# Kernel tuning notes

Hardware: AMD Instinct MI355X
Metric: run time of the kernel (lower is better)

Reference implementation:

```python
import jax, jax.numpy as jnp
import numpy as np

EPS = 1e-5

def _conv2d(x, w, b, pad):
    # NCHW conv, stride 1
    out = jax.lax.conv_general_dilated(x, w, (1, 1), [(pad, pad), (pad, pad)],
                                       dimension_numbers=('NCHW', 'OIHW', 'NCHW'))
    return out + b[None, :, None, None]

def _deform_conv2d(x, offset, mask, weight, bias, pad):
    # torchvision.ops.deform_conv2d (modulated, stride=1, dilation=1)
    B, C, H, W = x.shape
    O, _, K, _ = weight.shape
    kk = K * K
    off = offset.reshape(B, kk, 2, H, W)
    dy, dx = off[:, :, 0], off[:, :, 1]          # [B,kk,H,W]
    ki = (jnp.arange(kk) // K).astype(x.dtype)
    kj = (jnp.arange(kk) % K).astype(x.dtype)
    hh = jnp.arange(H, dtype=x.dtype)
    ww = jnp.arange(W, dtype=x.dtype)
    ys = dy + (hh[None, :, None] + ki[:, None, None] - pad)[None]  # [B,kk,H,W]
    xs = dx + (ww[None, None, :] + kj[:, None, None] - pad)[None]
    y0 = jnp.floor(ys); x0 = jnp.floor(xs)
    wy = ys - y0; wx = xs - x0
    xf = x.reshape(B, C, H * W)

    def gather(yi, xi):
        valid = ((yi >= 0) & (yi <= H - 1) & (xi >= 0) & (xi <= W - 1)).astype(x.dtype)
        yc = jnp.clip(yi, 0, H - 1).astype(jnp.int32)
        xc = jnp.clip(xi, 0, W - 1).astype(jnp.int32)
        idx = (yc * W + xc).reshape(B, -1)
        v = jax.vmap(lambda f, i: f[:, i])(xf, idx).reshape(B, C, kk, H, W)
        return v * valid[:, None]

    one = jnp.asarray(1.0, x.dtype)
    sampled = (gather(y0, x0) * ((one - wy) * (one - wx))[:, None]
               + gather(y0, x0 + 1) * ((one - wy) * wx)[:, None]
               + gather(y0 + 1, x0) * (wy * (one - wx))[:, None]
               + gather(y0 + 1, x0 + 1) * (wy * wx)[:, None])
    sampled = sampled * mask[:, None]            # modulation
    out = jnp.einsum('bckhw,ock->bohw', sampled, weight.reshape(O, C, kk))
    return out + bias[None, :, None, None]

def setup_inputs() -> dict:
    key = jax.random.key(0)
    ks = jax.random.split(key, 7)
    B, C, H, W = 8, 768, 32, 32
    x = jax.random.normal(ks[0], (B, C, H, W), jnp.float32)
    proj_w = jax.random.normal(ks[1], (768, 768, 3, 3), jnp.float32) * 0.02
    proj_b = jax.random.normal(ks[2], (768,), jnp.float32) * 0.02
    offset_w = jax.random.normal(ks[3], (18, 768, 3, 3), jnp.float32) * 0.01
    offset_b = jax.random.normal(ks[4], (18,), jnp.float32) * 0.01
    mask_w = jax.random.normal(ks[5], (9, 768, 3, 3), jnp.float32) * 0.01
    mask_b = jax.random.normal(ks[6], (9,), jnp.float32) * 0.01
    gamma = jnp.ones((768,), jnp.float32)
    beta = jnp.zeros((768,), jnp.float32)
    return {"x": x, "proj_w": proj_w, "proj_b": proj_b, "offset_w": offset_w,
            "offset_b": offset_b, "mask_w": mask_w, "mask_b": mask_b,
            "gamma": gamma, "beta": beta}

def reference(x, proj_w, proj_b, offset_w, offset_b, mask_w, mask_b, gamma, beta):
    pad = 1
    H, W = x.shape[-2], x.shape[-1]
    max_off = float(min(H, W) // 4)
    offset = jnp.clip(_conv2d(x, offset_w, offset_b, pad), -max_off, max_off)
    mask = 2.0 * jax.nn.sigmoid(_conv2d(x, mask_w, mask_b, pad))
    y = _deform_conv2d(x, offset, mask, proj_w, proj_b, pad)
    # SyncBatchNorm (training-mode batch statistics, biased var)
    mean = jnp.mean(y, axis=(0, 2, 3))
    var = jnp.var(y, axis=(0, 2, 3))
    yn = (y - mean[None, :, None, None]) * jax.lax.rsqrt(var + EPS)[None, :, None, None]
    yn = yn * gamma[None, :, None, None] + beta[None, :, None, None]
    return x + jax.nn.gelu(yn, approximate=False)
```

## Files before the change

### kernel.cpp

```cpp
#include <hip/hip_runtime.h>
#include <math.h>

typedef __attribute__((ext_vector_type(4))) float f32x4;
typedef __attribute__((ext_vector_type(8))) short s16x8;
typedef __attribute__((ext_vector_type(4))) unsigned int u32x4;
typedef unsigned short ushort_t;

#define HW   1024
#define C_IN 768
#define B_N  8

__device__ inline ushort_t f2bf(float f) {
    unsigned u = __builtin_bit_cast(unsigned, f);
    unsigned r = u + 0x7FFFu + ((u >> 16) & 1u);
    return (ushort_t)(r >> 16);
}
__device__ inline float bf2f(short s) {
    return __builtin_bit_cast(float, ((unsigned)(ushort_t)s) << 16);
}
__device__ inline void glds16(const void* g, void* l) {
    __builtin_amdgcn_global_load_lds(
        (const __attribute__((address_space(1))) unsigned*)g,
        (__attribute__((address_space(3))) unsigned*)l, 16, 0, 0);
}

__global__ __launch_bounds__(256) void prepack_xt(
    const float* __restrict__ x, ushort_t* __restrict__ xt)
{
    __shared__ ushort_t tile[64][66];
    int bid = blockIdx.x;
    int b  = bid / 192;
    int r  = bid % 192;
    int cg = r / 16, pg = r % 16;
    int c0 = cg * 64, p0 = pg * 64;
    int t = threadIdx.x;
#pragma unroll
    for (int i = 0; i < 16; ++i) {
        int idx = t + i * 256;
        int cr = idx >> 6, col = idx & 63;
        tile[cr][col] = f2bf(x[(((size_t)b * C_IN + c0 + cr) << 10) + p0 + col]);
    }
    __syncthreads();
#pragma unroll
    for (int i = 0; i < 16; ++i) {
        int idx = t + i * 256;
        int pr = idx >> 6, col = idx & 63;
        xt[((size_t)(b << 10) + p0 + pr) * C_IN + c0 + col] = tile[col][pr];
    }
}

__global__ __launch_bounds__(256) void prepack_proj(
    const float* __restrict__ pw, ushort_t* __restrict__ A)
{
    __shared__ ushort_t tile[16][584];
    int bid = blockIdx.x;
    int mf = bid / 12, cblk = bid - mf * 12;
    int t = threadIdx.x;
    const float* src = pw + (size_t)mf * 16 * 6912 + cblk * 576;
#pragma unroll
    for (int i = 0; i < 36; ++i) {
        int f = i * 256 + t;
        int orow = f / 576, col = f - orow * 576;
        tile[orow][col] = f2bf(src[(size_t)orow * 6912 + col]);
    }
    __syncthreads();
    int lane = t & 63, fi0 = t >> 6;
    for (int it = 0; it < 5; ++it) {
        int fidx = it * 4 + fi0;
        if (fidx < 18) {
            int tap = fidx >> 1, half = fidx & 1;
            int s = tap * 24 + cblk * 2 + half;
            int cl0 = half * 32 + ((lane >> 4) << 3);
            s16x8 pk;
#pragma unroll
            for (int e = 0; e < 8; ++e)
                pk[e] = (short)tile[lane & 15][(cl0 + e) * 9 + tap];
            *(s16x8*)(A + ((size_t)(s * 48 + mf) * 64 + lane) * 8) = pk;
        }
    }
}

__global__ __launch_bounds__(256) void prepack_om(
    const float* __restrict__ offw, const float* __restrict__ mskw,
    ushort_t* __restrict__ A2)
{
    int t = blockIdx.x * 256 + threadIdx.x;
    int lane = t & 63;
    int smi  = t >> 6;
    int s  = smi >> 1, mf = smi & 1;
    int oc = mf * 16 + (lane & 15);
    int k0 = s * 32 + ((lane >> 4) << 3);
    int tap = k0 / 768;
    int c   = k0 - tap * 768;
    s16x8 pk;
#pragma unroll
    for (int e = 0; e < 8; ++e) pk[e] = 0;
    if (oc < 27) {
        const float* src = (oc < 18)
            ? offw + ((size_t)oc        * 768 + c) * 9 + tap
            : mskw + ((size_t)(oc - 18) * 768 + c) * 9 + tap;
#pragma unroll
        for (int e = 0; e < 8; ++e) pk[e] = (short)f2bf(src[e * 9]);
    }
    *(s16x8*)(A2 + (size_t)smi * 512 + lane * 8) = pk;
}

__global__ __launch_bounds__(256) void offmask_mfma(
    const ushort_t* __restrict__ xt, const ushort_t* __restrict__ A2,
    const float* __restrict__ offb, const float* __restrict__ mbias,
    float* __restrict__ offs, float* __restrict__ maskb)
{
    int bid = blockIdx.x;
    int b = bid >> 5, pt = bid & 31;
    int p0 = pt << 5;
    int t = threadIdx.x, lane = t & 63, wv = t >> 6;
    int mf = wv >> 1, nf = wv & 1;
    int q = lane >> 4;
    int px = p0 + nf * 16 + (lane & 15);
    int h = px >> 5, w = px & 31;
    const char* xb = (const char*)xt + (size_t)b * (HW * 1536);
    f32x4 acc = (f32x4){0.f, 0.f, 0.f, 0.f};

    for (int tap = 0; tap < 9; ++tap) {
        int yy = h + tap / 3 - 1, xx = w + tap % 3 - 1;
        bool ok = (yy >= 0 && yy < 32 && xx >= 0 && xx < 32);
        int pos = ok ? (yy * 32 + xx) : 0;
        const char* bp = xb + (size_t)pos * 1536 + q * 16;
        for (int cs = 0; cs < 24; ++cs) {
            int s = tap * 24 + cs;
            s16x8 bf;
            if (ok) bf = *(const s16x8*)(bp + cs * 64);
            else    bf = (s16x8){0, 0, 0, 0, 0, 0, 0, 0};
            s16x8 af = *(const s16x8*)(A2 + ((size_t)(s * 2 + mf) * 64 + lane) * 8);
            acc = __builtin_amdgcn_mfma_f32_16x16x32_bf16(af, bf, acc, 0, 0, 0);
        }
    }
#pragma unroll
    for (int r = 0; r < 4; ++r) {
        int oc = mf * 16 + ((lane >> 4) << 2) + r;
        if (oc < 18) {
            float v = acc[r] + offb[oc];
            v = fminf(fmaxf(v, -8.f), 8.f);
            offs[((b * 18 + oc) << 10) + px] = v;
        } else if (oc < 27) {
            float v = acc[r] + mbias[oc - 18];
            maskb[((b * 9 + oc - 18) << 10) + px] = 2.f / (1.f + expf(-v));
        }
    }
}

__global__ __launch_bounds__(512) void sample_pack(
    const ushort_t* __restrict__ xt,
    const float* __restrict__ offs, const float* __restrict__ maskb,
    ushort_t* __restrict__ Bp)
{
    __shared__ float4 mw[9][16];
    __shared__ int4   mi[9][16];
    int bid = blockIdx.x;
    int b = bid >> 6, pxg = bid & 63;
    int px0 = pxg << 4;
    int t = threadIdx.x;

    if (t < 144) {
        int tap = t >> 4, pxl = t & 15;
        int px = px0 + pxl, h = px >> 5, w = px & 31;
        float dy = offs[((b * 18 + 2 * tap) << 10) + px];
        float dx = offs[((b * 18 + 2 * tap + 1) << 10) + px];
        float m  = maskb[((b * 9 + tap) << 10) + px];
        float ys = dy + (float)(h + tap / 3 - 1);
        float xs = dx + (float)(w + tap % 3 - 1);
        float fy = floorf(ys), fx = floorf(xs);
        float wy = ys - fy, wx = xs - fx;
        int iy0 = (int)fy, ix0 = (int)fx;
        int iy1 = iy0 + 1, ix1 = ix0 + 1;
        float vy0 = (iy0 >= 0 && iy0 < 32) ? 1.f : 0.f;
        float vy1 = (iy1 >= 0 && iy1 < 32) ? 1.f : 0.f;
        float vx0 = (ix0 >= 0 && ix0 < 32) ? 1.f : 0.f;
        float vx1 = (ix1 >= 0 && ix1 < 32) ? 1.f : 0.f;
        int cy0 = min(max(iy0, 0), 31), cx0 = min(max(ix0, 0), 31);
        int cy1 = min(max(iy1, 0), 31), cx1 = min(max(ix1, 0), 31);
        float4 wv4;
        wv4.x = (1.f - wy) * (1.f - wx) * m * vy0 * vx0;
        wv4.y = (1.f - wy) * wx         * m * vy0 * vx1;
        wv4.z = wy         * (1.f - wx) * m * vy1 * vx0;
        wv4.w = wy         * wx         * m * vy1 * vx1;
        mw[tap][pxl] = wv4;
        mi[tap][pxl] = make_int4((cy0 * 32 + cx0) * 1536, (cy0 * 32 + cx1) * 1536,
                                 (cy1 * 32 + cx0) * 1536, (cy1 * 32 + cx1) * 1536);
    }
    __syncthreads();

    int lane = t & 63, wv = t >> 6;
    int pxl = lane & 15, ko = lane >> 4;
    const char* xb = (const char*)xt + (size_t)b * (HW * 1536);

    for (int s = wv; s < 216; s += 8) {
        int tap = s / 24, cq = s - tap * 24;
        float4 w4 = mw[tap][pxl];
        int4  i4 = mi[tap][pxl];
        const char* base = xb + cq * 64 + ko * 16;
        s16x8 g0 = *(const s16x8*)(base + i4.x);
        s16x8 g1 = *(const s16x8*)(base + i4.y);
        s16x8 g2 = *(const s16x8*)(base + i4.z);
        s16x8 g3 = *(const s16x8*)(base + i4.w);
        u32x4 bw;
#pragma unroll
        for (int e2 = 0; e2 < 4; ++e2) {
            float v0 = w4.x * bf2f(g0[2 * e2])     + w4.y * bf2f(g1[2 * e2])
                     + w4.z * bf2f(g2[2 * e2])     + w4.w * bf2f(g3[2 * e2]);
            float v1 = w4.x * bf2f(g0[2 * e2 + 1]) + w4.y * bf2f(g1[2 * e2 + 1])
                     + w4.z * bf2f(g2[2 * e2 + 1]) + w4.w * bf2f(g3[2 * e2 + 1]);
            unsigned rr;
            asm("v_cvt_pk_bf16_f32 %0, %1, %2" : "=v"(rr) : "v"(v0), "v"(v1));
            bw[e2] = rr;
        }
        *(u32x4*)(Bp + ((size_t)(s * 8 + b) * 64 + pxg) * 512 + lane * 8) = bw;
    }
}

__global__ __launch_bounds__(1024, 2) void deform_gemm_lds2(
    const ushort_t* __restrict__ Amat, const ushort_t* __restrict__ Bp,
    float* __restrict__ y)
{
    __shared__ __align__(16) char Sbuf[4][20480];

    int id = blockIdx.x;
    int b = id & 7;
    int pxt = (id >> 3) & 7;
    int otile = id >> 6;
    int t = threadIdx.x, lane = t & 63, wv = t >> 6;
    int wm = wv >> 2, wn = wv & 3;

    f32x4 acc[3][2];
#pragma unroll
    for (int f = 0; f < 3; ++f)
#pragma unroll
        for (int n = 0; n < 2; ++n) acc[f][n] = (f32x4){0.f, 0.f, 0.f, 0.f};

#define CHUNK_SRC(c_, s_) ((c_) < 12                                         \
    ? (const char*)Amat + (((size_t)(s_) * 48 + otile * 12 + (c_)) << 10)    \
    : (const char*)Bp + ((((size_t)(s_) * 8 + b) * 64 + pxt * 8 + ((c_) - 12)) << 10))

#define STAGE(BUF, s_) do {                                                  \
    int c1_ = wv;                                                            \
    glds16(CHUNK_SRC(c1_, s_) + lane * 16, &Sbuf[BUF][c1_ << 10]);           \
    if (wv < 4) {                                                            \
        int c2_ = 16 + wv;                                                   \
        glds16(CHUNK_SRC(c2_, s_) + lane * 16, &Sbuf[BUF][c2_ << 10]);       \
    }                                                                        \
} while (0)

#define MFMA_PHASE(BUF) do {                                                 \
    const char* ab_ = &Sbuf[BUF][(wm * 3) << 10] + lane * 16;                \
    s16x8 a0_ = *(const s16x8*)(ab_);                                        \
    s16x8 a1_ = *(const s16x8*)(ab_ + 1024);                                 \
    s16x8 a2_ = *(const s16x8*)(ab_ + 2048);                                 \
    const char* bb_ = &Sbuf[BUF][(12 + wn * 2) << 10] + lane * 16;           \
    s16x8 b0_ = *(const s16x8*)(bb_);                                        \
    s16x8 b1_ = *(const s16x8*)(bb_ + 1024);                                 \
    acc[0][0] = __builtin_amdgcn_mfma_f32_16x16x32_bf16(a0_, b0_, acc[0][0], 0, 0, 0); \
    acc[0][1] = __builtin_amdgcn_mfma_f32_16x16x32_bf16(a0_, b1_, acc[0][1], 0, 0, 0); \
    acc[1][0] = __builtin_amdgcn_mfma_f32_16x16x32_bf16(a1_, b0_, acc[1][0], 0, 0, 0); \
    acc[1][1] = __builtin_amdgcn_mfma_f32_16x16x32_bf16(a1_, b1_, acc[1][1], 0, 0, 0); \
    acc[2][0] = __builtin_amdgcn_mfma_f32_16x16x32_bf16(a2_, b0_, acc[2][0], 0, 0, 0); \
    acc[2][1] = __builtin_amdgcn_mfma_f32_16x16x32_bf16(a2_, b1_, acc[2][1], 0, 0, 0); \
} while (0)

    STAGE(0, 0);
    STAGE(1, 1);

    for (int p = 0; p < 214; ++p) {
        int bufc = p & 3;
        STAGE((p + 2) & 3, p + 2);
        if (wv < 4) asm volatile("s_waitcnt vmcnt(4)" ::: "memory");
        else        asm volatile("s_waitcnt vmcnt(2)" ::: "memory");
        __builtin_amdgcn_s_barrier();
        __builtin_amdgcn_s_setprio(1);
        MFMA_PHASE(bufc);
        __builtin_amdgcn_s_setprio(0);
    }
    if (wv < 4) asm volatile("s_waitcnt vmcnt(2)" ::: "memory");
    else        asm volatile("s_waitcnt vmcnt(1)" ::: "memory");
    __builtin_amdgcn_s_barrier();
    MFMA_PHASE(214 & 3);
    asm volatile("s_waitcnt vmcnt(0)" ::: "memory");
    __builtin_amdgcn_s_barrier();
    MFMA_PHASE(215 & 3);

    int pxo = pxt * 128 + wn * 32 + (lane & 15);
    int obase = otile * 192 + wm * 48;
#pragma unroll
    for (int f = 0; f < 3; ++f) {
        int orow = obase + f * 16 + ((lane >> 4) << 2);
#pragma unroll
        for (int r = 0; r < 4; ++r) {
            size_t rowoff = ((size_t)(b * 768 + orow + r) << 10);
            y[rowoff + pxo]      = acc[f][0][r];
            y[rowoff + pxo + 16] = acc[f][1][r];
        }
    }
#undef CHUNK_SRC
#undef STAGE
#undef MFMA_PHASE
}

__global__ __launch_bounds__(512, 4) void deform_mfma_fused(
    const ushort_t* __restrict__ xt, const ushort_t* __restrict__ Amat,
    const float* __restrict__ offs, const float* __restrict__ maskb,
    float* __restrict__ y)
{
    __shared__ float4 meta_w[576];
    __shared__ int4   meta_i[576];
    __shared__ __align__(16) ushort_t Bs[2][64][64];

    int id = blockIdx.x;
    int b = id & 7;
    int pxt = (id >> 3) & 15;
    int otile = id >> 7;
    int p0 = pxt << 6;
    int t = threadIdx.x, lane = t & 63, wv = t >> 6;
    int wm = wv >> 1, wn = wv & 1;
    int q4 = lane >> 4;

    int bpx = wv * 8 + (lane >> 3);
    int oct = lane & 7;
    const int wchunk = (oct ^ (bpx & 7)) * 8;

    for (int i = t; i < 576; i += 512) {
        int k = i >> 6, j = i & 63;
        int hw = p0 + j, h = hw >> 5, w = hw & 31;
        float dy = offs[((b * 18 + 2 * k) << 10) + hw];
        float dx = offs[((b * 18 + 2 * k + 1) << 10) + hw];
        float m  = maskb[((b * 9 + k) << 10) + hw];
        float ys = dy + (float)(h + k / 3 - 1);
        float xs = dx + (float)(w + k % 3 - 1);
        float fy = floorf(ys), fx = floorf(xs);
        float wy = ys - fy, wx = xs - fx;
        int iy0 = (int)fy, ix0 = (int)fx;
        int iy1 = iy0 + 1, ix1 = ix0 + 1;
        float vy0 = (iy0 >= 0 && iy0 < 32) ? 1.f : 0.f;
        float vy1 = (iy1 >= 0 && iy1 < 32) ? 1.f : 0.f;
        float vx0 = (ix0 >= 0 && ix0 < 32) ? 1.f : 0.f;
        float vx1 = (ix1 >= 0 && ix1 < 32) ? 1.f : 0.f;
        int cy0 = min(max(iy0, 0), 31), cx0 = min(max(ix0, 0), 31);
        int cy1 = min(max(iy1, 0), 31), cx1 = min(max(ix1, 0), 31);
        float4 wv4;
        wv4.x = (1.f - wy) * (1.f - wx) * m * vy0 * vx0;
        wv4.y = (1.f - wy) * wx         * m * vy0 * vx1;
        wv4.z = wy         * (1.f - wx) * m * vy1 * vx0;
        wv4.w = wy         * wx         * m * vy1 * vx1;
        meta_w[i] = wv4;
        meta_i[i] = make_int4((cy0 * 32 + cx0) * 1536, (cy0 * 32 + cx1) * 1536,
                              (cy1 * 32 + cx0) * 1536, (cy1 * 32 + cx1) * 1536);
    }
    asm volatile("s_waitcnt lgkmcnt(0)" ::: "memory");
    __builtin_amdgcn_s_barrier();

    f32x4 acc[3][2];
#pragma unroll
    for (int f = 0; f < 3; ++f)
#pragma unroll
        for (int n = 0; n < 2; ++n) acc[f][n] = (f32x4){0.f, 0.f, 0.f, 0.f};

    const char* xb = (const char*)xt + (size_t)b * (HW * 1536);
    const int afrag0 = otile * 12 + wm * 3;

    s16x8 ga0, ga1, ga2, ga3, gb0, gb1, gb2, gb3;
    float4 w4a, w4b;

#define WBAR() do { asm volatile("s_waitcnt lgkmcnt(0)" ::: "memory"); \
                    __builtin_amdgcn_s_barrier(); } while (0)
#define ISSUE(G0, G1, G2, G3, W4, qq) do {                                  \
    int nt_ = (qq) / 12, nc_ = (qq) - nt_ * 12;                             \
    W4 = meta_w[nt_ * 64 + bpx];                                            \
    int4 i4_ = meta_i[nt_ * 64 + bpx];                                      \
    const char* bsrc_ = xb + nc_ * 128 + oct * 16;                          \
    G0 = *(const s16x8*)(bsrc_ + i4_.x);                                    \
    G1 = *(const s16x8*)(bsrc_ + i4_.y);                                    \
    G2 = *(const s16x8*)(bsrc_ + i4_.z);                                    \
    G3 = *(const s16x8*)(bsrc_ + i4_.w);                                    \
} while (0)
#define BUILD(G0, G1, G2, G3, W4, BUF) do {                                 \
    u32x4 bw_;                                                              \
    _Pragma("unroll")                                                       \
    for (int e2 = 0; e2 < 4; ++e2) {                                        \
        float v0_ = W4.x * bf2f(G0[2*e2])   + W4.y * bf2f(G1[2*e2])         \
                  + W4.z * bf2f(G2[2*e2])   + W4.w * bf2f(G3[2*e2]);        \
        float v1_ = W4.x * bf2f(G0[2*e2+1]) + W4.y * bf2f(G1[2*e2+1])       \
                  + W4.z * bf2f(G2[2*e2+1]) + W4.w * bf2f(G3[2*e2+1]);      \
        unsigned rr_;                                                       \
        asm("v_cvt_pk_bf16_f32 %0, %1, %2" : "=v"(rr_) : "v"(v0_), "v"(v1_)); \
        bw_[e2] = rr_;                                                      \
    }                                                                       \
    *(u32x4*)&Bs[BUF][bpx][wchunk] = bw_;                                   \
} while (0)
#define MFMA_PHASE_F(P, BUF) do {                                           \
    _Pragma("unroll")                                                       \
    for (int kk = 0; kk < 2; ++kk) {                                        \
        int s_ = 2 * (P) + kk;                                              \
        const s16x8* ap_ = (const s16x8*)(Amat +                            \
            ((size_t)(s_ * 48 + afrag0) * 64 + lane) * 8);                  \
        s16x8 a0_ = ap_[0], a1_ = ap_[64], a2_ = ap_[128];                  \
        int rc_ = ((kk * 4 + q4) ^ (lane & 7)) * 8;                         \
        s16x8 b0_ = *(const s16x8*)&Bs[BUF][wn * 32 + (lane & 15)][rc_];    \
        s16x8 b1_ = *(const s16x8*)&Bs[BUF][wn * 32 + 16 + (lane & 15)][rc_]; \
        acc[0][0] = __builtin_amdgcn_mfma_f32_16x16x32_bf16(a0_, b0_, acc[0][0], 0, 0, 0); \
        acc[0][1] = __builtin_amdgcn_mfma_f32_16x16x32_bf16(a0_, b1_, acc[0][1], 0, 0, 0); \
        acc[1][0] = __builtin_amdgcn_mfma_f32_16x16x32_bf16(a1_, b0_, acc[1][0], 0, 0, 0); \
        acc[1][1] = __builtin_amdgcn_mfma_f32_16x16x32_bf16(a1_, b1_, acc[1][1], 0, 0, 0); \
        acc[2][0] = __builtin_amdgcn_mfma_f32_16x16x32_bf16(a2_, b0_, acc[2][0], 0, 0, 0); \
        acc[2][1] = __builtin_amdgcn_mfma_f32_16x16x32_bf16(a2_, b1_, acc[2][1], 0, 0, 0); \
    }                                                                       \
} while (0)

    ISSUE(ga0, ga1, ga2, ga3, w4a, 0);
    ISSUE(gb0, gb1, gb2, gb3, w4b, 1);
    BUILD(ga0, ga1, ga2, ga3, w4a, 0);
    WBAR();
    for (int pp = 0; pp < 54; ++pp) {
        int pe = 2 * pp;
        if (pp < 53) ISSUE(ga0, ga1, ga2, ga3, w4a, pe + 2);
        MFMA_PHASE_F(pe, 0);
        BUILD(gb0, gb1, gb2, gb3, w4b, 1);
        WBAR();
        int po = pe + 1;
        if (pp < 53) ISSUE(gb0, gb1, gb2, gb3, w4b, po + 2);
        MFMA_PHASE_F(po, 1);
        if (pp < 53) BUILD(ga0, ga1, ga2, ga3, w4a, 0);
        WBAR();
    }
    int pxo = p0 + wn * 32 + (lane & 15);
    int obase = otile * 192 + wm * 48;
#pragma unroll
    for (int f = 0; f < 3; ++f) {
        int orow = obase + f * 16 + ((lane >> 4) << 2);
#pragma unroll
        for (int r = 0; r < 4; ++r) {
            size_t rowoff = ((size_t)(b * 768 + orow + r) << 10);
            y[rowoff + pxo]      = acc[f][0][r];
            y[rowoff + pxo + 16] = acc[f][1][r];
        }
    }
#undef WBAR
#undef ISSUE
#undef BUILD
#undef MFMA_PHASE_F
}

__global__ __launch_bounds__(256) void stats_kernel(
    const float* __restrict__ y, float* __restrict__ stats)
{
    int o = blockIdx.x;
    int tid = threadIdx.x;
    float s1 = 0.f, s2 = 0.f;
    for (int i = tid; i < B_N * HW; i += 256) {
        int b = i >> 10, hw = i & 1023;
        float v = y[(((size_t)b * 768 + o) << 10) + hw];
        s1 += v; s2 += v * v;
    }
#pragma unroll
    for (int off = 32; off > 0; off >>= 1) {
        s1 += __shfl_down(s1, off);
        s2 += __shfl_down(s2, off);
    }
    __shared__ float ls1[4], ls2[4];
    int wid = tid >> 6, lane = tid & 63;
    if (lane == 0) { ls1[wid] = s1; ls2[wid] = s2; }
    __syncthreads();
    if (tid == 0) {
        float t1 = ls1[0] + ls1[1] + ls1[2] + ls1[3];
        float t2 = ls2[0] + ls2[1] + ls2[2] + ls2[3];
        float mean = t1 * (1.0f / 8192.0f);
        float var  = t2 * (1.0f / 8192.0f) - mean * mean;
        stats[o]       = mean;
        stats[768 + o] = 1.0f / sqrtf(var + 1e-5f);
    }
}

__global__ __launch_bounds__(256) void finalize_kernel(
    const float* __restrict__ x, const float* __restrict__ stats,
    const float* __restrict__ gamma, const float* __restrict__ beta,
    float* __restrict__ y)
{
    const int total4 = B_N * 768 * HW / 4;
    for (int f = blockIdx.x * 256 + threadIdx.x; f < total4;
         f += gridDim.x * 256) {
        int e = f << 2;
        int o = (e >> 10) % 768;
        float mean = stats[o], rstd = stats[768 + o];
        float ga = gamma[o], be = beta[o];
        float4 v  = ((const float4*)y)[f];
        float4 xv = ((const float4*)x)[f];
        float4 r;
        {
            float yn = (v.x - mean) * rstd * ga + be;
            r.x = xv.x + 0.5f * yn * (1.0f + erff(yn * 0.70710678f));
        }
        {
            float yn = (v.y - mean) * rstd * ga + be;
            r.y = xv.y + 0.5f * yn * (1.0f + erff(yn * 0.70710678f));
        }
        {
            float yn = (v.z - mean) * rstd * ga + be;
            r.z = xv.z + 0.5f * yn * (1.0f + erff(yn * 0.70710678f));
        }
        {
            float yn = (v.w - mean) * rstd * ga + be;
            r.w = xv.w + 0.5f * yn * (1.0f + erff(yn * 0.70710678f));
        }
        ((float4*)y)[f] = r;
    }
}

extern "C" void kernel_launch(void* const* d_in, const int* in_sizes, int n_in,
                              void* d_out, int out_size, void* d_ws, size_t ws_size,
                              hipStream_t stream)
{
    const float* x        = (const float*)d_in[0];
    const float* proj_w   = (const float*)d_in[1];
    const float* offset_w = (const float*)d_in[3];
    const float* offset_b = (const float*)d_in[4];
    const float* mask_w   = (const float*)d_in[5];
    const float* mask_b   = (const float*)d_in[6];
    const float* gamma    = (const float*)d_in[7];
    const float* beta     = (const float*)d_in[8];

    char* ws = (char*)d_ws;
    float*    offs  = (float*)(ws);
    float*    maskb = (float*)(ws + 589824);
    float*    stats = (float*)(ws + 884736);
    ushort_t* A     = (ushort_t*)(ws + 890880);
    ushort_t* A2    = (ushort_t*)(ws + 11507712);
    ushort_t* xt    = (ushort_t*)(ws + 11950080);
    ushort_t* Bp    = (ushort_t*)(ws + 24532992);
    float* y = (float*)d_out;

    const size_t NEED_SPLIT = 24532992ull + 113246208ull;

    prepack_xt<<<1536, 256, 0, stream>>>(x, xt);
    prepack_om<<<108, 256, 0, stream>>>(offset_w, mask_w, A2);
    prepack_proj<<<576, 256, 0, stream>>>(proj_w, A);
    offmask_mfma<<<256, 256, 0, stream>>>(xt, A2, offset_b, mask_b, offs, maskb);

    if (ws_size >= NEED_SPLIT) {
        sample_pack<<<512, 512, 0, stream>>>(xt, offs, maskb, Bp);
        deform_gemm_lds2<<<256, 1024, 0, stream>>>(A, Bp, y);
    } else {
        deform_mfma_fused<<<512, 512, 0, stream>>>(xt, A, offs, maskb, y);
    }

    stats_kernel<<<768, 256, 0, stream>>>(y, stats);
    finalize_kernel<<<2048, 256, 0, stream>>>(x, stats, gamma, beta, y);
}
```

Measured before the change: 255.8 us.

## Fuse BN stats into GEMM epilogue, split-K offset conv, retile deform GEMM

The deform GEMM epilogue now reduces per-channel sum and sum-of-squares across lanes and accumulates them with atomics. This removes the separate stats pass that re-read all of y, and mean/rstd are now computed in finalize. The offset/mask conv uses 16 waves with a 4-way split-K and an LDS reduction, giving it more parallelism. The GEMM is retiled to 512-thread blocks with a doubled grid, and sample_pack's block ordering interleaves batches. The trade-off is atomic contention, an extra memset, and float atomics that make the summation order nondeterministic.

```diff
diff --git a/kernel.cpp b/kernel.cpp
--- a/kernel.cpp
+++ b/kernel.cpp
@@ -105,46 +105,55 @@
     *(s16x8*)(A2 + (size_t)smi * 512 + lane * 8) = pk;
 }
 
-__global__ __launch_bounds__(256) void offmask_mfma(
+__global__ __launch_bounds__(1024) void offmask_mfma(
     const ushort_t* __restrict__ xt, const ushort_t* __restrict__ A2,
     const float* __restrict__ offb, const float* __restrict__ mbias,
     float* __restrict__ offs, float* __restrict__ maskb)
 {
+    __shared__ f32x4 red[16][64];
     int bid = blockIdx.x;
     int b = bid >> 5, pt = bid & 31;
     int p0 = pt << 5;
     int t = threadIdx.x, lane = t & 63, wv = t >> 6;
-    int mf = wv >> 1, nf = wv & 1;
+    int kq = wv >> 2, quad = wv & 3;
+    int mf = quad >> 1, nf = quad & 1;
     int q = lane >> 4;
     int px = p0 + nf * 16 + (lane & 15);
     int h = px >> 5, w = px & 31;
     const char* xb = (const char*)xt + (size_t)b * (HW * 1536);
     f32x4 acc = (f32x4){0.f, 0.f, 0.f, 0.f};
 
-    for (int tap = 0; tap < 9; ++tap) {
+    int s0 = kq * 54;
+    for (int s = s0; s < s0 + 54; ++s) {
+        int tap = s / 24, cs = s - tap * 24;
         int yy = h + tap / 3 - 1, xx = w + tap % 3 - 1;
         bool ok = (yy >= 0 && yy < 32 && xx >= 0 && xx < 32);
         int pos = ok ? (yy * 32 + xx) : 0;
-        const char* bp = xb + (size_t)pos * 1536 + q * 16;
-        for (int cs = 0; cs < 24; ++cs) {
-            int s = tap * 24 + cs;
-            s16x8 bf;
-            if (ok) bf = *(const s16x8*)(bp + cs * 64);
-            else    bf = (s16x8){0, 0, 0, 0, 0, 0, 0, 0};
-            s16x8 af = *(const s16x8*)(A2 + ((size_t)(s * 2 + mf) * 64 + lane) * 8);
-            acc = __builtin_amdgcn_mfma_f32_16x16x32_bf16(af, bf, acc, 0, 0, 0);
-        }
-    }
-#pragma unroll
-    for (int r = 0; r < 4; ++r) {
-        int oc = mf * 16 + ((lane >> 4) << 2) + r;
-        if (oc < 18) {
-            float v = acc[r] + offb[oc];
-            v = fminf(fmaxf(v, -8.f), 8.f);
-            offs[((b * 18 + oc) << 10) + px] = v;
-        } else if (oc < 27) {
-            float v = acc[r] + mbias[oc - 18];
-            maskb[((b * 9 + oc - 18) << 10) + px] = 2.f / (1.f + expf(-v));
+        const char* bp = xb + (size_t)pos * 1536 + cs * 64 + q * 16;
+        s16x8 bf;
+        if (ok) bf = *(const s16x8*)bp;
+        else    bf = (s16x8){0, 0, 0, 0, 0, 0, 0, 0};
+        s16x8 af = *(const s16x8*)(A2 + ((size_t)(s * 2 + mf) * 64 + lane) * 8);
+        acc = __builtin_amdgcn_mfma_f32_16x16x32_bf16(af, bf, acc, 0, 0, 0);
+    }
+    red[wv][lane] = acc;
+    __syncthreads();
+    if (wv < 4) {
+        f32x4 r1 = red[wv + 4][lane];
+        f32x4 r2 = red[wv + 8][lane];
+        f32x4 r3 = red[wv + 12][lane];
+        acc += r1; acc += r2; acc += r3;
+#pragma unroll
+        for (int r = 0; r < 4; ++r) {
+            int oc = mf * 16 + ((lane >> 4) << 2) + r;
+            if (oc < 18) {
+                float v = acc[r] + offb[oc];
+                v = fminf(fmaxf(v, -8.f), 8.f);
+                offs[((b * 18 + oc) << 10) + px] = v;
+            } else if (oc < 27) {
+                float v = acc[r] + mbias[oc - 18];
+                maskb[((b * 9 + oc - 18) << 10) + px] = 2.f / (1.f + expf(-v));
+            }
         }
     }
 }
@@ -157,7 +166,7 @@
     __shared__ float4 mw[9][16];
     __shared__ int4   mi[9][16];
     int bid = blockIdx.x;
-    int b = bid >> 6, pxg = bid & 63;
+    int b = bid & 7, pxg = bid >> 3;
     int px0 = pxg << 4;
     int t = threadIdx.x;
 
@@ -218,18 +227,19 @@
     }
 }
 
-__global__ __launch_bounds__(1024, 2) void deform_gemm_lds2(
+__global__ __launch_bounds__(512, 4) void deform_gemm_lds4(
     const ushort_t* __restrict__ Amat, const ushort_t* __restrict__ Bp,
-    float* __restrict__ y)
-{
-    __shared__ __align__(16) char Sbuf[4][20480];
+    float* __restrict__ y, float* __restrict__ stats)
+{
+    __shared__ __align__(16) char Sbuf[4][16384];
 
     int id = blockIdx.x;
     int b = id & 7;
-    int pxt = (id >> 3) & 7;
-    int otile = id >> 6;
+    int pxt = (id >> 3) & 15;
+    int otile = id >> 7;
+    int p0 = pxt << 6;
     int t = threadIdx.x, lane = t & 63, wv = t >> 6;
-    int wm = wv >> 2, wn = wv & 3;
+    int wm = wv >> 1, wn = wv & 1;
 
     f32x4 acc[3][2];
 #pragma unroll
@@ -237,16 +247,14 @@
 #pragma unroll
         for (int n = 0; n < 2; ++n) acc[f][n] = (f32x4){0.f, 0.f, 0.f, 0.f};
 
-#define CHUNK_SRC(c_, s_) ((c_) < 12                                         \
-    ? (const char*)Amat + (((size_t)(s_) * 48 + otile * 12 + (c_)) << 10)    \
-    : (const char*)Bp + ((((size_t)(s_) * 8 + b) * 64 + pxt * 8 + ((c_) - 12)) << 10))
-
 #define STAGE(BUF, s_) do {                                                  \
-    int c1_ = wv;                                                            \
-    glds16(CHUNK_SRC(c1_, s_) + lane * 16, &Sbuf[BUF][c1_ << 10]);           \
-    if (wv < 4) {                                                            \
-        int c2_ = 16 + wv;                                                   \
-        glds16(CHUNK_SRC(c2_, s_) + lane * 16, &Sbuf[BUF][c2_ << 10]);       \
+    _Pragma("unroll")                                                        \
+    for (int i_ = 0; i_ < 2; ++i_) {                                         \
+        int c_ = wv * 2 + i_;                                                \
+        const char* src_ = (c_ < 12)                                         \
+            ? (const char*)Amat + (((size_t)(s_) * 48 + otile * 12 + c_) << 10) \
+            : (const char*)Bp + ((((size_t)(s_) * 8 + b) * 64 + pxt * 4 + (c_ - 12)) << 10); \
+        glds16(src_ + lane * 16, &Sbuf[BUF][c_ << 10]);                      \
     }                                                                        \
 } while (0)
 
@@ -270,36 +278,44 @@
     STAGE(1, 1);
 
     for (int p = 0; p < 214; ++p) {
-        int bufc = p & 3;
         STAGE((p + 2) & 3, p + 2);
-        if (wv < 4) asm volatile("s_waitcnt vmcnt(4)" ::: "memory");
-        else        asm volatile("s_waitcnt vmcnt(2)" ::: "memory");
+        asm volatile("s_waitcnt vmcnt(4)" ::: "memory");
         __builtin_amdgcn_s_barrier();
         __builtin_amdgcn_s_setprio(1);
-        MFMA_PHASE(bufc);
+        MFMA_PHASE(p & 3);
         __builtin_amdgcn_s_setprio(0);
     }
-    if (wv < 4) asm volatile("s_waitcnt vmcnt(2)" ::: "memory");
-    else        asm volatile("s_waitcnt vmcnt(1)" ::: "memory");
+    asm volatile("s_waitcnt vmcnt(2)" ::: "memory");
     __builtin_amdgcn_s_barrier();
     MFMA_PHASE(214 & 3);
     asm volatile("s_waitcnt vmcnt(0)" ::: "memory");
     __builtin_amdgcn_s_barrier();
     MFMA_PHASE(215 & 3);
 
-    int pxo = pxt * 128 + wn * 32 + (lane & 15);
+    int pxo = p0 + wn * 32 + (lane & 15);
     int obase = otile * 192 + wm * 48;
 #pragma unroll
     for (int f = 0; f < 3; ++f) {
         int orow = obase + f * 16 + ((lane >> 4) << 2);
 #pragma unroll
         for (int r = 0; r < 4; ++r) {
+            float a = acc[f][0][r], c = acc[f][1][r];
             size_t rowoff = ((size_t)(b * 768 + orow + r) << 10);
-            y[rowoff + pxo]      = acc[f][0][r];
-            y[rowoff + pxo + 16] = acc[f][1][r];
-        }
-    }
-#undef CHUNK_SRC
+            y[rowoff + pxo]      = a;
+            y[rowoff + pxo + 16] = c;
+            float s1 = a + c;
+            float s2 = a * a + c * c;
+#pragma unroll
+            for (int m = 1; m < 16; m <<= 1) {
+                s1 += __shfl_xor(s1, m);
+                s2 += __shfl_xor(s2, m);
+            }
+            if ((lane & 15) == 0) {
+                atomicAdd(&stats[orow + r], s1);
+                atomicAdd(&stats[768 + orow + r], s2);
+            }
+        }
+    }
 #undef STAGE
 #undef MFMA_PHASE
 }
@@ -468,12 +484,8 @@
     if (lane == 0) { ls1[wid] = s1; ls2[wid] = s2; }
     __syncthreads();
     if (tid == 0) {
-        float t1 = ls1[0] + ls1[1] + ls1[2] + ls1[3];
-        float t2 = ls2[0] + ls2[1] + ls2[2] + ls2[3];
-        float mean = t1 * (1.0f / 8192.0f);
-        float var  = t2 * (1.0f / 8192.0f) - mean * mean;
-        stats[o]       = mean;
-        stats[768 + o] = 1.0f / sqrtf(var + 1e-5f);
+        stats[o]       = ls1[0] + ls1[1] + ls1[2] + ls1[3];
+        stats[768 + o] = ls2[0] + ls2[1] + ls2[2] + ls2[3];
     }
 }
 
@@ -487,7 +499,10 @@
          f += gridDim.x * 256) {
         int e = f << 2;
         int o = (e >> 10) % 768;
-        float mean = stats[o], rstd = stats[768 + o];
+        float s1 = stats[o], s2 = stats[768 + o];
+        float mean = s1 * (1.0f / 8192.0f);
+        float var  = s2 * (1.0f / 8192.0f) - mean * mean;
+        float rstd = 1.0f / sqrtf(var + 1e-5f);
         float ga = gamma[o], be = beta[o];
         float4 v  = ((const float4*)y)[f];
         float4 xv = ((const float4*)x)[f];
@@ -540,15 +555,16 @@
     prepack_xt<<<1536, 256, 0, stream>>>(x, xt);
     prepack_om<<<108, 256, 0, stream>>>(offset_w, mask_w, A2);
     prepack_proj<<<576, 256, 0, stream>>>(proj_w, A);
-    offmask_mfma<<<256, 256, 0, stream>>>(xt, A2, offset_b, mask_b, offs, maskb);
+    offmask_mfma<<<256, 1024, 0, stream>>>(xt, A2, offset_b, mask_b, offs, maskb);
 
     if (ws_size >= NEED_SPLIT) {
+        hipMemsetAsync(stats, 0, 1536 * sizeof(float), stream);
         sample_pack<<<512, 512, 0, stream>>>(xt, offs, maskb, Bp);
-        deform_gemm_lds2<<<256, 1024, 0, stream>>>(A, Bp, y);
+        deform_gemm_lds4<<<512, 512, 0, stream>>>(A, Bp, y, stats);
     } else {
         deform_mfma_fused<<<512, 512, 0, stream>>>(xt, A, offs, maskb, y);
-    }
-
-    stats_kernel<<<768, 256, 0, stream>>>(y, stats);
+        stats_kernel<<<768, 256, 0, stream>>>(y, stats);
+    }
+
     finalize_kernel<<<2048, 256, 0, stream>>>(x, stats, gamma, beta, y);
 }
```

After: 251.5 us. About the same (-1.7%).
